# Optimization experiments

Measured on AMD Instinct MI355X. Metric: run time of the kernel, lower is better.

Reference implementation:

```python
import jax, jax.numpy as jnp
import numpy as np

LN_EPS = 1e-5

def _layernorm(x, g, b):
    mu = jnp.mean(x, axis=-1, keepdims=True)
    var = jnp.var(x, axis=-1, keepdims=True)
    return (x - mu) * jax.lax.rsqrt(var + LN_EPS) * g + b

def setup_inputs() -> dict:
    key = jax.random.key(0)
    ks = jax.random.split(key, 16)
    B, N, dim, dim_out, H = 4, 8192, 128, 256, 4
    hd = dim_out // H
    s = 0.02
    inp = {
        "xyz": jax.random.normal(ks[0], (B, N, 3), jnp.float32),
        "features": jax.random.normal(ks[1], (B, N, dim), jnp.float32),
        "Wq": s * jax.random.normal(ks[2], (dim, dim_out), jnp.float32),
        "bq": jnp.zeros((dim_out,), jnp.float32),
        "Wk": s * jax.random.normal(ks[3], (dim, dim_out), jnp.float32),
        "bk": jnp.zeros((dim_out,), jnp.float32),
        "Wv": s * jax.random.normal(ks[4], (dim, dim_out), jnp.float32),
        "bv": jnp.zeros((dim_out,), jnp.float32),
        "Wp1": s * jax.random.normal(ks[5], (3, hd), jnp.float32),
        "bp1": jnp.zeros((hd,), jnp.float32),
        "Wp2": s * jax.random.normal(ks[6], (hd, hd), jnp.float32),
        "bp2": jnp.zeros((hd,), jnp.float32),
        "Wf1": s * jax.random.normal(ks[7], (dim_out, dim_out), jnp.float32),
        "bf1": jnp.zeros((dim_out,), jnp.float32),
        "Wf2": s * jax.random.normal(ks[8], (dim_out, dim_out), jnp.float32),
        "bf2": jnp.zeros((dim_out,), jnp.float32),
        "g1": jnp.ones((dim,), jnp.float32),
        "b1": jnp.zeros((dim,), jnp.float32),
        "g2": jnp.ones((dim_out,), jnp.float32),
        "b2": jnp.zeros((dim_out,), jnp.float32),
    }
    return inp

def reference(xyz, features, Wq, bq, Wk, bk, Wv, bv, Wp1, bp1, Wp2, bp2,
              Wf1, bf1, Wf2, bf2, g1, b1, g2, b2):
    B, N, _ = xyz.shape
    K = 16
    H = 4
    dim_out = Wq.shape[1]
    hd = dim_out // H

    # KNN via squared pairwise distances (same ordering as torch.cdist)
    sqn = jnp.sum(xyz * xyz, axis=-1)                       # (B,N)
    d2 = sqn[:, :, None] + sqn[:, None, :] - 2.0 * jnp.einsum('bnd,bmd->bnm', xyz, xyz)
    _, knn_idx = jax.lax.top_k(-d2, K)                      # (B,N,K) smallest dists

    bidx = jnp.arange(B)[:, None, None]
    neighbor_xyz = xyz[bidx, knn_idx]                       # (B,N,K,3)
    relative_pos = neighbor_xyz - xyz[:, :, None, :]        # (B,N,K,3)

    # positional encoding MLP: 3 -> hd -> hd
    pos = jax.nn.relu(relative_pos @ Wp1 + bp1) @ Wp2 + bp2 # (B,N,K,hd)

    q = (features @ Wq + bq).reshape(B, N, H, hd)           # (B,N,H,hd)
    nbr_feat = features[bidx, knn_idx]                      # (B,N,K,dim)
    k = (nbr_feat @ Wk + bk).reshape(B, N, K, H, hd)
    v = (nbr_feat @ Wv + bv).reshape(B, N, K, H, hd)

    pos_b = pos[:, :, :, None, :]                           # (B,N,K,1,hd)
    attn = jnp.sum(q[:, :, None, :, :] * (k + pos_b), axis=-1) / jnp.sqrt(jnp.float32(hd))  # (B,N,K,H)
    attn = jax.nn.softmax(attn, axis=2)                     # softmax over neighbors

    out = jnp.sum(attn[..., None] * (v + pos_b), axis=2)    # (B,N,H,hd)
    out = out.reshape(B, N, dim_out)

    fc = jax.nn.relu(out @ Wf1 + bf1) @ Wf2 + bf2
    out = _layernorm(fc, g2, b2) + (_layernorm(features, g1, b1) @ Wq + bq)

    attn_out = jnp.transpose(attn, (0, 3, 1, 2))            # (B,H,N,K) as torch
    return out, attn_out
```

## Files before the change

### kernel.cpp

```cpp
#include <hip/hip_runtime.h>
#include <hip/hip_bf16.h>
#include <math.h>

typedef __hip_bfloat16 bf16;
typedef __attribute__((ext_vector_type(8))) short short8v;
typedef __attribute__((ext_vector_type(4))) float f32x4;

#define NBATCH 4
#define NPTS   8192
#define TOTPTS 32768
#define DIM    128
#define DOUT   256
#define KNN    16

__device__ __forceinline__ float b2f(bf16 x) { return __bfloat162float(x); }
__device__ __forceinline__ bf16 f2b(float x) { return __float2bfloat16(x); }

__device__ __forceinline__ float rsum32(float v) {
#pragma unroll
  for (int o = 16; o; o >>= 1) v += __shfl_down(v, o, 32);
  return v;
}

__global__ __launch_bounds__(256) void pack_kernel(const float* __restrict__ xyz,
                                                   float4* __restrict__ xyzw) {
  const int p = blockIdx.x * 256 + threadIdx.x;
  const float x = xyz[3 * p], y = xyz[3 * p + 1], z = xyz[3 * p + 2];
  xyzw[p] = make_float4(x, y, z, x * x + y * y + z * z);
}

template <int S>
__device__ __forceinline__ void ins16(float d2, int g, int lane, int seg,
                                      float& bd, int& bi, float& tmax) {
  unsigned long long mask = __ballot(d2 < tmax);
  while (mask) {
    const int l = __builtin_ctzll(mask);
    mask &= mask - 1;
    const float dl = __int_as_float(
        __builtin_amdgcn_readlane(__float_as_int(d2), l));
    if (dl < tmax) {
      const int il = g + l;
      const bool keep = bd <= dl;
      const float pd = __shfl_up(bd, 1, 16);
      const int   pi = __shfl_up(bi, 1, 16);
      const bool fromPrev = ((lane & 15) > 0) && (pd > dl);
      const float nbd = keep ? bd : (fromPrev ? pd : dl);
      const int   nbi = keep ? bi : (fromPrev ? pi : il);
      bd = (seg == S) ? nbd : bd;
      bi = (seg == S) ? nbi : bi;
      tmax = __int_as_float(
          __builtin_amdgcn_readlane(__float_as_int(bd), S * 16 + 15));
    }
  }
}

__global__ __launch_bounds__(256) void knn_wave_kernel(
    const float4* __restrict__ xyzw, unsigned short* __restrict__ knn_out) {
  const int wid  = threadIdx.x >> 6;
  const int lane = threadIdx.x & 63;
  const int seg  = lane >> 4;
  const int q0 = (blockIdx.x * 4 + wid) * 4;
  const int b = q0 >> 13;
  const float4* cb = xyzw + (size_t)b * NPTS;

  const float4 mA = xyzw[q0 + 0];
  const float4 mB = xyzw[q0 + 1];
  const float4 mC = xyzw[q0 + 2];
  const float4 mD = xyzw[q0 + 3];

  float bd = INFINITY;
  int   bi = 0x7fff;
  float tA = INFINITY, tB = INFINITY, tC = INFINITY, tD = INFINITY;

  for (int g = 0; g < NPTS; g += 64) {
    const float4 t = cb[g + lane];
    const float dA = mA.w + t.w - 2.f * (mA.x * t.x + mA.y * t.y + mA.z * t.z);
    const float dB = mB.w + t.w - 2.f * (mB.x * t.x + mB.y * t.y + mB.z * t.z);
    const float dC = mC.w + t.w - 2.f * (mC.x * t.x + mC.y * t.y + mC.z * t.z);
    const float dD = mD.w + t.w - 2.f * (mD.x * t.x + mD.y * t.y + mD.z * t.z);
    ins16<0>(dA, g, lane, seg, bd, bi, tA);
    ins16<1>(dB, g, lane, seg, bd, bi, tB);
    ins16<2>(dC, g, lane, seg, bd, bi, tC);
    ins16<3>(dD, g, lane, seg, bd, bi, tD);
  }
  knn_out[(size_t)q0 * KNN + lane] = (unsigned short)bi;
}

__global__ __launch_bounds__(256) void pos_kernel(
    const float4* __restrict__ xyzw, const unsigned short* __restrict__ knn_in,
    const float* __restrict__ Wp1, const float* __restrict__ bp1,
    const float* __restrict__ Wp2, const float* __restrict__ bp2,
    bf16* __restrict__ posG) {
  __shared__ float h1S[4][16][64];
  const int wid = threadIdx.x >> 6, lane = threadIdx.x & 63;
  const int p = blockIdx.x * 4 + wid;
  const int b = p >> 13, n = p & (NPTS - 1);
  const float4* cb = xyzw + (size_t)b * NPTS;
  const float4 me = cb[n];

  float rx = 0.f, ry = 0.f, rz = 0.f;
  if (lane < 16) {
    const int idx = knn_in[(size_t)p * KNN + lane];
    const float4 t = cb[idx];
    rx = t.x - me.x; ry = t.y - me.y; rz = t.z - me.z;
  }
  const float w0 = Wp1[lane], w1 = Wp1[64 + lane], w2 = Wp1[128 + lane];
  const float bb1 = bp1[lane], bb2 = bp2[lane];
#pragma unroll
  for (int k = 0; k < 16; k++) {
    const float r0 = __shfl(rx, k, 64);
    const float r1 = __shfl(ry, k, 64);
    const float r2 = __shfl(rz, k, 64);
    h1S[wid][k][lane] = fmaxf(bb1 + r0 * w0 + r1 * w1 + r2 * w2, 0.f);
  }
  __syncthreads();

  float acc[16];
#pragma unroll
  for (int k = 0; k < 16; k++) acc[k] = bb2;
  for (int jq = 0; jq < 16; jq++) {
    const float w2a = Wp2[(jq * 4 + 0) * 64 + lane];
    const float w2b = Wp2[(jq * 4 + 1) * 64 + lane];
    const float w2c = Wp2[(jq * 4 + 2) * 64 + lane];
    const float w2d = Wp2[(jq * 4 + 3) * 64 + lane];
#pragma unroll
    for (int k = 0; k < 16; k++) {
      const float4 h = *(const float4*)&h1S[wid][k][jq * 4];
      acc[k] += h.x * w2a + h.y * w2b + h.z * w2c + h.w * w2d;
    }
  }
#pragma unroll
  for (int k = 0; k < 16; k++)
    posG[((size_t)p * KNN + k) * 64 + lane] = f2b(acc[k]);
}

__global__ __launch_bounds__(256) void proj_kernel(
    const float* __restrict__ feat,
    const float* __restrict__ Wq, const float* __restrict__ bq,
    const float* __restrict__ Wk, const float* __restrict__ bk,
    const float* __restrict__ Wv, const float* __restrict__ bv,
    const float* __restrict__ g1, const float* __restrict__ b1,
    bf16* __restrict__ Q, bf16* __restrict__ Kf, bf16* __restrict__ Vf,
    float* __restrict__ skip) {
  __shared__ float f[8][DIM];
  __shared__ float ln[8][DIM];
  __shared__ float mu8[8], rs8[8];
  const int tid = threadIdx.x;
  const size_t r0 = (size_t)blockIdx.x * 8;
  const float* src = feat + r0 * DIM;
#pragma unroll
  for (int i = 0; i < 4; i++) {
    const int idx = tid + i * 256;
    f[idx >> 7][idx & 127] = src[idx];
  }
  __syncthreads();
  const int r = tid >> 5, j = tid & 31;
  const float a0 = f[r][j], a1 = f[r][j + 32], a2 = f[r][j + 64], a3 = f[r][j + 96];
  float s = rsum32(a0 + a1 + a2 + a3);
  if (!j) mu8[r] = s * (1.f / 128.f);
  __syncthreads();
  const float mu = mu8[r];
  const float d0 = a0 - mu, d1 = a1 - mu, d2 = a2 - mu, d3 = a3 - mu;
  float ss = rsum32(d0 * d0 + d1 * d1 + d2 * d2 + d3 * d3);
  if (!j) rs8[r] = rsqrtf(ss * (1.f / 128.f) + 1e-5f);
  __syncthreads();
  const float rsd = rs8[r];
  ln[r][j]      = d0 * rsd * g1[j]      + b1[j];
  ln[r][j + 32] = d1 * rsd * g1[j + 32] + b1[j + 32];
  ln[r][j + 64] = d2 * rsd * g1[j + 64] + b1[j + 64];
  ln[r][j + 96] = d3 * rsd * g1[j + 96] + b1[j + 96];
  __syncthreads();
  float qa[8] = {}, ka[8] = {}, va[8] = {}, sa[8] = {};
  for (int d = 0; d < DIM; d += 4) {
    const float wq0 = Wq[(d + 0) * DOUT + tid], wq1 = Wq[(d + 1) * DOUT + tid];
    const float wq2 = Wq[(d + 2) * DOUT + tid], wq3 = Wq[(d + 3) * DOUT + tid];
    const float wk0 = Wk[(d + 0) * DOUT + tid], wk1 = Wk[(d + 1) * DOUT + tid];
    const float wk2 = Wk[(d + 2) * DOUT + tid], wk3 = Wk[(d + 3) * DOUT + tid];
    const float wv0 = Wv[(d + 0) * DOUT + tid], wv1 = Wv[(d + 1) * DOUT + tid];
    const float wv2 = Wv[(d + 2) * DOUT + tid], wv3 = Wv[(d + 3) * DOUT + tid];
#pragma unroll
    for (int rr = 0; rr < 8; rr++) {
      const float4 fv = *(const float4*)&f[rr][d];
      const float4 lv = *(const float4*)&ln[rr][d];
      qa[rr] += fv.x * wq0 + fv.y * wq1 + fv.z * wq2 + fv.w * wq3;
      ka[rr] += fv.x * wk0 + fv.y * wk1 + fv.z * wk2 + fv.w * wk3;
      va[rr] += fv.x * wv0 + fv.y * wv1 + fv.z * wv2 + fv.w * wv3;
      sa[rr] += lv.x * wq0 + lv.y * wq1 + lv.z * wq2 + lv.w * wq3;
    }
  }
  const float bqv = bq[tid], bkv = bk[tid], bvv = bv[tid];
#pragma unroll
  for (int rr = 0; rr < 8; rr++) {
    const size_t o = (r0 + rr) * DOUT + tid;
    Q[o]    = f2b(qa[rr] + bqv);
    Kf[o]   = f2b(ka[rr] + bkv);
    Vf[o]   = f2b(va[rr] + bvv);
    skip[o] = sa[rr] + bqv;
  }
}

__global__ __launch_bounds__(256) void attn_kernel(
    const unsigned short* __restrict__ knn_in,
    bf16* __restrict__ QOA, const bf16* __restrict__ Kf, const bf16* __restrict__ Vf,
    const bf16* __restrict__ posG,
    float* __restrict__ AOUT) {
  __shared__ int nidxS[16];
  const int tid  = threadIdx.x;
  const int w    = tid >> 6;
  const int lane = tid & 63;
  const int p = blockIdx.x;
  const int b = p >> 13, n = p & (NPTS - 1);

  if (tid < 16) nidxS[tid] = knn_in[(size_t)p * KNN + tid];
  const float qreg = b2f(QOA[(size_t)p * DOUT + tid]);
  __syncthreads();

  float kreg[16], vreg[16], posr[16];
  const size_t rowbase = (size_t)b * NPTS;
  const bf16* pg = posG + (size_t)p * KNN * 64 + lane;
#pragma unroll
  for (int k = 0; k < 16; k++) {
    const size_t row = (rowbase + (size_t)nidxS[k]) * DOUT + tid;
    kreg[k] = b2f(Kf[row]);
    vreg[k] = b2f(Vf[row]);
    posr[k] = b2f(pg[k * 64]);
  }

  float lg[16];
#pragma unroll
  for (int k = 0; k < 16; k++) lg[k] = qreg * (kreg[k] + posr[k]);
#pragma unroll
  for (int o = 32; o; o >>= 1) {
#pragma unroll
    for (int k = 0; k < 16; k++) lg[k] += __shfl_xor(lg[k], o, 64);
  }
  float m = -INFINITY;
#pragma unroll
  for (int k = 0; k < 16; k++) { lg[k] *= 0.125f; m = fmaxf(m, lg[k]); }
  float sum = 0.f;
#pragma unroll
  for (int k = 0; k < 16; k++) { lg[k] = expf(lg[k] - m); sum += lg[k]; }
  const float inv = 1.f / sum;
#pragma unroll
  for (int k = 0; k < 16; k++) lg[k] *= inv;
  float av = 0.f;
#pragma unroll
  for (int k = 0; k < 16; k++) if (lane == k) av = lg[k];
  if (lane < 16)
    AOUT[(((size_t)b * 4 + w) * NPTS + n) * KNN + lane] = av;
  float o = 0.f;
#pragma unroll
  for (int k = 0; k < 16; k++) o += lg[k] * (vreg[k] + posr[k]);
  QOA[(size_t)p * DOUT + tid] = f2b(o);
}

__global__ __launch_bounds__(256) void wprep_kernel(
    const float* __restrict__ Wf1, const float* __restrict__ Wf2,
    bf16* __restrict__ Wt1, bf16* __restrict__ Wt2) {
  const int t = blockIdx.x * 256 + threadIdx.x;
  const float* src = (t & 8192) ? Wf2 : Wf1;
  bf16*        dst = (t & 8192) ? Wt2 : Wt1;
  const int rem = t & 8191;
  const int c = rem >> 5, k8 = (rem & 31) * 8;
#pragma unroll
  for (int j = 0; j < 8; j++)
    dst[c * 256 + k8 + j] = f2b(src[(k8 + j) * 256 + c]);
}

#define FRB 16
#define FCP 264
__global__ __launch_bounds__(256) void ffn_kernel(
    const bf16* __restrict__ OA,
    const bf16* __restrict__ Wt1, const float* __restrict__ bf1,
    const bf16* __restrict__ Wt2, const float* __restrict__ bf2,
    const float* __restrict__ g2, const float* __restrict__ b2p,
    float* __restrict__ out) {
  __shared__ float zs[FRB][FCP];
  __shared__ float mu16[FRB], rs16[FRB];
  bf16* base = (bf16*)&zs[0][0];
  const int ysoff = FRB * FCP;
  const int tid  = threadIdx.x;
  const int w    = tid >> 6;
  const int lane = tid & 63;
  const int g    = lane >> 4, lr = lane & 15;
  const int cw   = w * 64;
  const size_t r0 = (size_t)blockIdx.x * FRB;

  {
    const short8v* src = (const short8v*)(OA + r0 * DOUT);
#pragma unroll
    for (int i = 0; i < 2; i++) {
      const int ch = tid + i * 256;
      const int row = ch >> 5, c8 = (ch & 31) * 8;
      *(short8v*)&base[row * FCP + c8] = src[ch];
    }
  }
  __syncthreads();

  f32x4 a0 = {0.f, 0.f, 0.f, 0.f}, a1 = a0, a2 = a0, a3 = a0;

#define GEMM8(OFF, WT)                                                         \
  _Pragma("unroll")                                                            \
  for (int s = 0; s < 8; s++) {                                                \
    const int k0 = s * 32 + g * 8;                                             \
    const short8v av = *(const short8v*)&base[(OFF) + lr * FCP + k0];          \
    a0 = __builtin_amdgcn_mfma_f32_16x16x32_bf16(                              \
        av, *(const short8v*)&(WT)[(cw +  0 + lr) * 256 + k0], a0, 0, 0, 0);   \
    a1 = __builtin_amdgcn_mfma_f32_16x16x32_bf16(                              \
        av, *(const short8v*)&(WT)[(cw + 16 + lr) * 256 + k0], a1, 0, 0, 0);   \
    a2 = __builtin_amdgcn_mfma_f32_16x16x32_bf16(                              \
        av, *(const short8v*)&(WT)[(cw + 32 + lr) * 256 + k0], a2, 0, 0, 0);   \
    a3 = __builtin_amdgcn_mfma_f32_16x16x32_bf16(                              \
        av, *(const short8v*)&(WT)[(cw + 48 + lr) * 256 + k0], a3, 0, 0, 0);   \
  }

  GEMM8(0, Wt1)

#define STORE_Y(ACC, T)                                                        \
  {                                                                            \
    const int c = cw + 16 * (T) + lr;                                          \
    const float bb = bf1[c];                                                   \
    _Pragma("unroll")                                                          \
    for (int e = 0; e < 4; e++)                                                \
      base[ysoff + (4 * g + e) * FCP + c] = f2b(fmaxf(ACC[e] + bb, 0.f));      \
  }
  STORE_Y(a0, 0) STORE_Y(a1, 1) STORE_Y(a2, 2) STORE_Y(a3, 3)
  __syncthreads();

  a0 = (f32x4){0.f, 0.f, 0.f, 0.f}; a1 = a0; a2 = a0; a3 = a0;
  GEMM8(ysoff, Wt2)
  __syncthreads();

#define STORE_Z(ACC, T)                                                        \
  {                                                                            \
    const int c = cw + 16 * (T) + lr;                                          \
    const float bb = bf2[c];                                                   \
    _Pragma("unroll")                                                          \
    for (int e = 0; e < 4; e++) zs[4 * g + e][c] = ACC[e] + bb;                \
  }
  STORE_Z(a0, 0) STORE_Z(a1, 1) STORE_Z(a2, 2) STORE_Z(a3, 3)
  __syncthreads();

  const int r = tid >> 4, j = tid & 15;
  float s = 0.f;
#pragma unroll
  for (int k2 = 0; k2 < 16; k2++) s += zs[r][j + 16 * k2];
#pragma unroll
  for (int o = 8; o; o >>= 1) s += __shfl_down(s, o, 16);
  if (!j) mu16[r] = s * (1.f / 256.f);
  __syncthreads();
  const float mu = mu16[r];
  float ss = 0.f;
#pragma unroll
  for (int k2 = 0; k2 < 16; k2++) { const float dd = zs[r][j + 16 * k2] - mu; ss += dd * dd; }
#pragma unroll
  for (int o = 8; o; o >>= 1) ss += __shfl_down(ss, o, 16);
  if (!j) rs16[r] = rsqrtf(ss * (1.f / 256.f) + 1e-5f);
  __syncthreads();

  const float gv = g2[tid], bbv = b2p[tid];
#pragma unroll
  for (int rr = 0; rr < FRB; rr++) {
    const size_t o = (r0 + rr) * DOUT + tid;
    const float sk = out[o];
    out[o] = (zs[rr][tid] - mu16[rr]) * rs16[rr] * gv + bbv + sk;
  }
}

extern "C" void kernel_launch(void* const* d_in, const int* in_sizes, int n_in,
                              void* d_out, int out_size, void* d_ws, size_t ws_size,
                              hipStream_t stream) {
  const float* xyz  = (const float*)d_in[0];
  const float* feat = (const float*)d_in[1];
  const float* Wq   = (const float*)d_in[2];
  const float* bq   = (const float*)d_in[3];
  const float* Wk   = (const float*)d_in[4];
  const float* bk   = (const float*)d_in[5];
  const float* Wv   = (const float*)d_in[6];
  const float* bv   = (const float*)d_in[7];
  const float* Wp1  = (const float*)d_in[8];
  const float* bp1  = (const float*)d_in[9];
  const float* Wp2  = (const float*)d_in[10];
  const float* bp2  = (const float*)d_in[11];
  const float* Wf1  = (const float*)d_in[12];
  const float* bf1  = (const float*)d_in[13];
  const float* Wf2  = (const float*)d_in[14];
  const float* bf2  = (const float*)d_in[15];
  const float* g1   = (const float*)d_in[16];
  const float* b1   = (const float*)d_in[17];
  const float* g2   = (const float*)d_in[18];
  const float* b2   = (const float*)d_in[19];

  float* out  = (float*)d_out;
  float* aout = out + (size_t)TOTPTS * DOUT;

  unsigned short* knn  = (unsigned short*)d_ws;
  float4*         xyzw = (float4*)aout;
  bf16* QOA  = (bf16*)((char*)d_ws + (size_t)(1 << 20));
  bf16* Kf   = QOA + (size_t)TOTPTS * DOUT;
  bf16* Vf   = Kf  + (size_t)TOTPTS * DOUT;
  bf16* posG = (bf16*)((char*)d_ws + (size_t)(49 << 20));
  bf16* Wt1  = Kf;
  bf16* Wt2  = Kf + 65536;

  pack_kernel<<<TOTPTS / 256, 256, 0, stream>>>(xyz, xyzw);
  knn_wave_kernel<<<TOTPTS / 16, 256, 0, stream>>>(xyzw, knn);
  pos_kernel<<<TOTPTS / 4, 256, 0, stream>>>(xyzw, knn, Wp1, bp1, Wp2, bp2, posG);
  proj_kernel<<<TOTPTS / 8, 256, 0, stream>>>(feat, Wq, bq, Wk, bk, Wv, bv, g1, b1,
                                              QOA, Kf, Vf, out);
  attn_kernel<<<TOTPTS, 256, 0, stream>>>(knn, QOA, Kf, Vf, posG, aout);
  wprep_kernel<<<64, 256, 0, stream>>>(Wf1, Wf2, Wt1, Wt2);
  ffn_kernel<<<TOTPTS / FRB, 256, 0, stream>>>(QOA, Wt1, bf1, Wt2, bf2, g2, b2, out);
}
```

Before: 735.4 us.

## Move QKV and skip projection onto bf16 MFMA with hi/lo split precision

Replaces the scalar FP32 projection of features onto Wq, Wk, Wv (and the layernormed skip path) with MFMA 16x16x32 bf16 instructions. Both operands are split into high and low bf16 parts, and three MFMAs per product keep the result close to fp32. A new prep kernel converts and transposes the weights into split bf16 buffers stored in scratch space in the attention-output region. Rows per block go from 8 to 16. This trades extra MFMA work and weight-prep traffic for removing the FP32 FMA bottleneck of the old proj_kernel.

```diff
diff --git a/kernel.cpp b/kernel.cpp
--- a/kernel.cpp
+++ b/kernel.cpp
@@ -134,68 +134,136 @@
     posG[((size_t)p * KNN + k) * 64 + lane] = f2b(acc[k]);
 }
 
+__global__ __launch_bounds__(256) void wprep_qkv_kernel(
+    const float* __restrict__ Wq, const float* __restrict__ Wk,
+    const float* __restrict__ Wv,
+    bf16* __restrict__ Wqh, bf16* __restrict__ Wql,
+    bf16* __restrict__ Wkh, bf16* __restrict__ Wkl,
+    bf16* __restrict__ Wvh, bf16* __restrict__ Wvl) {
+  const int t = blockIdx.x * 256 + threadIdx.x;
+  const int m = t >> 12;
+  const int rem = t & 4095;
+  const int c = rem >> 4, k8 = (rem & 15) * 8;
+  const float* src = (m == 0) ? Wq : (m == 1) ? Wk : Wv;
+  bf16* dh = (m == 0) ? Wqh : (m == 1) ? Wkh : Wvh;
+  bf16* dl = (m == 0) ? Wql : (m == 1) ? Wkl : Wvl;
+#pragma unroll
+  for (int j = 0; j < 8; j++) {
+    const float x = src[(k8 + j) * 256 + c];
+    const bf16 hi = f2b(x);
+    dh[c * 128 + k8 + j] = hi;
+    dl[c * 128 + k8 + j] = f2b(x - b2f(hi));
+  }
+}
+
+#define PR  16
+#define PCP 136
 __global__ __launch_bounds__(256) void proj_kernel(
     const float* __restrict__ feat,
-    const float* __restrict__ Wq, const float* __restrict__ bq,
-    const float* __restrict__ Wk, const float* __restrict__ bk,
-    const float* __restrict__ Wv, const float* __restrict__ bv,
+    const bf16* __restrict__ Wqh, const bf16* __restrict__ Wql,
+    const bf16* __restrict__ Wkh, const bf16* __restrict__ Wkl,
+    const bf16* __restrict__ Wvh, const bf16* __restrict__ Wvl,
+    const float* __restrict__ bq, const float* __restrict__ bk,
+    const float* __restrict__ bv,
     const float* __restrict__ g1, const float* __restrict__ b1,
     bf16* __restrict__ Q, bf16* __restrict__ Kf, bf16* __restrict__ Vf,
     float* __restrict__ skip) {
-  __shared__ float f[8][DIM];
-  __shared__ float ln[8][DIM];
-  __shared__ float mu8[8], rs8[8];
-  const int tid = threadIdx.x;
-  const size_t r0 = (size_t)blockIdx.x * 8;
-  const float* src = feat + r0 * DIM;
-#pragma unroll
-  for (int i = 0; i < 4; i++) {
-    const int idx = tid + i * 256;
-    f[idx >> 7][idx & 127] = src[idx];
-  }
-  __syncthreads();
-  const int r = tid >> 5, j = tid & 31;
-  const float a0 = f[r][j], a1 = f[r][j + 32], a2 = f[r][j + 64], a3 = f[r][j + 96];
-  float s = rsum32(a0 + a1 + a2 + a3);
-  if (!j) mu8[r] = s * (1.f / 128.f);
-  __syncthreads();
-  const float mu = mu8[r];
-  const float d0 = a0 - mu, d1 = a1 - mu, d2 = a2 - mu, d3 = a3 - mu;
-  float ss = rsum32(d0 * d0 + d1 * d1 + d2 * d2 + d3 * d3);
-  if (!j) rs8[r] = rsqrtf(ss * (1.f / 128.f) + 1e-5f);
-  __syncthreads();
-  const float rsd = rs8[r];
-  ln[r][j]      = d0 * rsd * g1[j]      + b1[j];
-  ln[r][j + 32] = d1 * rsd * g1[j + 32] + b1[j + 32];
-  ln[r][j + 64] = d2 * rsd * g1[j + 64] + b1[j + 64];
-  ln[r][j + 96] = d3 * rsd * g1[j + 96] + b1[j + 96];
-  __syncthreads();
-  float qa[8] = {}, ka[8] = {}, va[8] = {}, sa[8] = {};
-  for (int d = 0; d < DIM; d += 4) {
-    const float wq0 = Wq[(d + 0) * DOUT + tid], wq1 = Wq[(d + 1) * DOUT + tid];
-    const float wq2 = Wq[(d + 2) * DOUT + tid], wq3 = Wq[(d + 3) * DOUT + tid];
-    const float wk0 = Wk[(d + 0) * DOUT + tid], wk1 = Wk[(d + 1) * DOUT + tid];
-    const float wk2 = Wk[(d + 2) * DOUT + tid], wk3 = Wk[(d + 3) * DOUT + tid];
-    const float wv0 = Wv[(d + 0) * DOUT + tid], wv1 = Wv[(d + 1) * DOUT + tid];
-    const float wv2 = Wv[(d + 2) * DOUT + tid], wv3 = Wv[(d + 3) * DOUT + tid];
-#pragma unroll
-    for (int rr = 0; rr < 8; rr++) {
-      const float4 fv = *(const float4*)&f[rr][d];
-      const float4 lv = *(const float4*)&ln[rr][d];
-      qa[rr] += fv.x * wq0 + fv.y * wq1 + fv.z * wq2 + fv.w * wq3;
-      ka[rr] += fv.x * wk0 + fv.y * wk1 + fv.z * wk2 + fv.w * wk3;
-      va[rr] += fv.x * wv0 + fv.y * wv1 + fv.z * wv2 + fv.w * wv3;
-      sa[rr] += lv.x * wq0 + lv.y * wq1 + lv.z * wq2 + lv.w * wq3;
-    }
-  }
-  const float bqv = bq[tid], bkv = bk[tid], bvv = bv[tid];
-#pragma unroll
-  for (int rr = 0; rr < 8; rr++) {
-    const size_t o = (r0 + rr) * DOUT + tid;
-    Q[o]    = f2b(qa[rr] + bqv);
-    Kf[o]   = f2b(ka[rr] + bkv);
-    Vf[o]   = f2b(va[rr] + bvv);
-    skip[o] = sa[rr] + bqv;
+  __shared__ float fS[PR][DIM];
+  __shared__ bf16 fh[PR][PCP], fl[PR][PCP];
+  __shared__ bf16 lh[PR][PCP], ll[PR][PCP];
+  const int tid  = threadIdx.x;
+  const size_t r0 = (size_t)blockIdx.x * PR;
+
+  {
+    const float4* src = (const float4*)(feat + r0 * DIM);
+    float4* dst = (float4*)&fS[0][0];
+#pragma unroll
+    for (int i = 0; i < 2; i++) dst[tid + i * 256] = src[tid + i * 256];
+  }
+  __syncthreads();
+
+  {
+    const int r = tid >> 4, j = tid & 15;
+    float v[8];
+    float s = 0.f;
+#pragma unroll
+    for (int i = 0; i < 8; i++) { v[i] = fS[r][j * 8 + i]; s += v[i]; }
+#pragma unroll
+    for (int o = 8; o; o >>= 1) s += __shfl_down(s, o, 16);
+    const float mu = __shfl(s, 0, 16) * (1.f / 128.f);
+    float ss = 0.f;
+#pragma unroll
+    for (int i = 0; i < 8; i++) { const float d = v[i] - mu; ss += d * d; }
+#pragma unroll
+    for (int o = 8; o; o >>= 1) ss += __shfl_down(ss, o, 16);
+    const float rsd = rsqrtf(__shfl(ss, 0, 16) * (1.f / 128.f) + 1e-5f);
+#pragma unroll
+    for (int i = 0; i < 8; i++) {
+      const int c = j * 8 + i;
+      const bf16 hv = f2b(v[i]);
+      fh[r][c] = hv;
+      fl[r][c] = f2b(v[i] - b2f(hv));
+      const float lnv = (v[i] - mu) * rsd * g1[c] + b1[c];
+      const bf16 lhv = f2b(lnv);
+      lh[r][c] = lhv;
+      ll[r][c] = f2b(lnv - b2f(lhv));
+    }
+  }
+  __syncthreads();
+
+  const int w    = tid >> 6;
+  const int lane = tid & 63;
+  const int g    = lane >> 4, lr = lane & 15;
+  const int cw   = w * 64;
+  f32x4 qa[4], ka[4], va[4], sa[4];
+#pragma unroll
+  for (int t = 0; t < 4; t++) {
+    qa[t] = (f32x4){0.f, 0.f, 0.f, 0.f};
+    ka[t] = qa[t]; va[t] = qa[t]; sa[t] = qa[t];
+  }
+#pragma unroll
+  for (int s = 0; s < 4; s++) {
+    const int k0 = s * 32 + g * 8;
+    const short8v ah = *(const short8v*)&fh[lr][k0];
+    const short8v al = *(const short8v*)&fl[lr][k0];
+    const short8v nh = *(const short8v*)&lh[lr][k0];
+    const short8v nl = *(const short8v*)&ll[lr][k0];
+#pragma unroll
+    for (int t = 0; t < 4; t++) {
+      const int c = cw + 16 * t + lr;
+      const short8v wqh = *(const short8v*)&Wqh[c * 128 + k0];
+      const short8v wql = *(const short8v*)&Wql[c * 128 + k0];
+      const short8v wkh = *(const short8v*)&Wkh[c * 128 + k0];
+      const short8v wkl = *(const short8v*)&Wkl[c * 128 + k0];
+      const short8v wvh = *(const short8v*)&Wvh[c * 128 + k0];
+      const short8v wvl = *(const short8v*)&Wvl[c * 128 + k0];
+      qa[t] = __builtin_amdgcn_mfma_f32_16x16x32_bf16(ah, wqh, qa[t], 0, 0, 0);
+      qa[t] = __builtin_amdgcn_mfma_f32_16x16x32_bf16(ah, wql, qa[t], 0, 0, 0);
+      qa[t] = __builtin_amdgcn_mfma_f32_16x16x32_bf16(al, wqh, qa[t], 0, 0, 0);
+      ka[t] = __builtin_amdgcn_mfma_f32_16x16x32_bf16(ah, wkh, ka[t], 0, 0, 0);
+      ka[t] = __builtin_amdgcn_mfma_f32_16x16x32_bf16(ah, wkl, ka[t], 0, 0, 0);
+      ka[t] = __builtin_amdgcn_mfma_f32_16x16x32_bf16(al, wkh, ka[t], 0, 0, 0);
+      va[t] = __builtin_amdgcn_mfma_f32_16x16x32_bf16(ah, wvh, va[t], 0, 0, 0);
+      va[t] = __builtin_amdgcn_mfma_f32_16x16x32_bf16(ah, wvl, va[t], 0, 0, 0);
+      va[t] = __builtin_amdgcn_mfma_f32_16x16x32_bf16(al, wvh, va[t], 0, 0, 0);
+      sa[t] = __builtin_amdgcn_mfma_f32_16x16x32_bf16(nh, wqh, sa[t], 0, 0, 0);
+      sa[t] = __builtin_amdgcn_mfma_f32_16x16x32_bf16(nh, wql, sa[t], 0, 0, 0);
+      sa[t] = __builtin_amdgcn_mfma_f32_16x16x32_bf16(nl, wqh, sa[t], 0, 0, 0);
+    }
+  }
+
+#pragma unroll
+  for (int t = 0; t < 4; t++) {
+    const int c = cw + 16 * t + lr;
+    const float bqv = bq[c], bkv = bk[c], bvv = bv[c];
+#pragma unroll
+    for (int e = 0; e < 4; e++) {
+      const size_t o = (r0 + 4 * g + e) * DOUT + c;
+      Q[o]    = f2b(qa[t][e] + bqv);
+      Kf[o]   = f2b(ka[t][e] + bkv);
+      Vf[o]   = f2b(va[t][e] + bvv);
+      skip[o] = sa[t][e] + bqv;
+    }
   }
 }
 
@@ -402,12 +470,20 @@
   bf16* posG = (bf16*)((char*)d_ws + (size_t)(49 << 20));
   bf16* Wt1  = Kf;
   bf16* Wt2  = Kf + 65536;
+  bf16* Wqh  = (bf16*)((char*)aout + (512 << 10));
+  bf16* Wql  = Wqh + 32768;
+  bf16* Wkh  = Wql + 32768;
+  bf16* Wkl  = Wkh + 32768;
+  bf16* Wvh  = Wkl + 32768;
+  bf16* Wvl  = Wvh + 32768;
 
   pack_kernel<<<TOTPTS / 256, 256, 0, stream>>>(xyz, xyzw);
+  wprep_qkv_kernel<<<48, 256, 0, stream>>>(Wq, Wk, Wv, Wqh, Wql, Wkh, Wkl, Wvh, Wvl);
   knn_wave_kernel<<<TOTPTS / 16, 256, 0, stream>>>(xyzw, knn);
   pos_kernel<<<TOTPTS / 4, 256, 0, stream>>>(xyzw, knn, Wp1, bp1, Wp2, bp2, posG);
-  proj_kernel<<<TOTPTS / 8, 256, 0, stream>>>(feat, Wq, bq, Wk, bk, Wv, bv, g1, b1,
-                                              QOA, Kf, Vf, out);
+  proj_kernel<<<TOTPTS / PR, 256, 0, stream>>>(feat, Wqh, Wql, Wkh, Wkl, Wvh, Wvl,
+                                               bq, bk, bv, g1, b1,
+                                               QOA, Kf, Vf, out);
   attn_kernel<<<TOTPTS, 256, 0, stream>>>(knn, QOA, Kf, Vf, posG, aout);
   wprep_kernel<<<64, 256, 0, stream>>>(Wf1, Wf2, Wt1, Wt2);
   ffn_kernel<<<TOTPTS / FRB, 256, 0, stream>>>(QOA, Wt1, bf1, Wt2, bf2, g2, b2, out);
```

New measurement: 684.3 us. 7.0% less time.
